# Optimization experiments

Measured on AMD Instinct MI355X. Metric: run time of the kernel, lower is better.

Reference implementation:

```python
import jax, jax.numpy as jnp
import numpy as np

D_MODEL = 512
KERNEL = 16
DILATIONS = (1, 1, 2, 2, 4, 4, 8, 8)
HEADS = len(DILATIONS)
HEAD_W = D_MODEL // HEADS
B, L = 2, 1024
MODE = "forward"  # causal: window sees only prior words


def setup_inputs() -> dict:
    key = jax.random.key(0)
    ks = jax.random.split(key, 8)
    s = 0.02  # small init like nn.Linear
    return {
        "tensor": jax.random.normal(ks[0], (B, L, D_MODEL), jnp.float32),
        "Wq": jax.random.normal(ks[1], (HEADS, HEAD_W, D_MODEL), jnp.float32) * s,
        "bq": jnp.zeros((HEADS, HEAD_W), jnp.float32),
        "Wk": jax.random.normal(ks[2], (HEADS, KERNEL, HEAD_W, D_MODEL), jnp.float32) * s,
        "bk": jnp.zeros((HEADS, KERNEL, HEAD_W), jnp.float32),
        "Wv": jax.random.normal(ks[3], (HEADS, KERNEL, HEAD_W, D_MODEL), jnp.float32) * s,
        "bv": jnp.zeros((HEADS, KERNEL, HEAD_W), jnp.float32),
        "Wo": jax.random.normal(ks[4], (D_MODEL, HEADS, HEAD_W), jnp.float32) * s,
        "bo": jnp.zeros((D_MODEL,), jnp.float32),
    }


def _window_indices():
    """Static gather indices replicating Glimpses.dilocal's dilated unfold.

    Returns idx of shape (H, L, K) indexing into a sequence zero-padded by
    max_off on both sides: content[h, l, k] = x_padded[idx[h, l, k]].
    """
    dil = np.asarray(DILATIONS)  # (H,)
    max_off = int((KERNEL - 1) * dil.max())
    if MODE == "forward":
        front = (KERNEL - 1) * dil           # all padding in front (causal)
    elif MODE == "backward":
        front = np.zeros_like(dil)           # all padding behind
    else:  # center
        front = ((KERNEL - 1) * dil) // 2
    l = np.arange(L)[None, :, None]
    k = np.arange(KERNEL)[None, None, :]
    d = dil[:, None, None]
    f = front[:, None, None]
    idx = l + k * d - f + max_off            # (H, L, K), always in-range
    return jnp.asarray(idx), max_off


_IDX, _MOFF = _window_indices()


def reference(tensor, Wq, bq, Wk, bk, Wv, bv, Wo, bo):
    # tensor: (B, L, D)
    xp = jnp.pad(tensor, ((0, 0), (_MOFF, _MOFF), (0, 0)))
    content = xp[:, _IDX, :]                                   # (B,H,L,K,D)
    # per-head query projection (kernel position 1)
    q = jnp.einsum('bld,hod->bhlo', tensor, Wq) + bq[:, None, :]        # (B,H,L,hw)
    # per-(head, kernel-position) independent key/value projections
    k = jnp.einsum('bhlkd,hkod->bhlko', content, Wk) + bk[:, None, :, :]
    v = jnp.einsum('bhlkd,hkod->bhlko', content, Wv) + bv[:, None, :, :]
    # tiny local attention over the K window positions
    logits = jnp.einsum('bhlo,bhlko->bhlk', q, k)               # (B,H,L,K)
    score = jax.nn.softmax(logits, axis=-1)
    # NOTE: original scales AFTER the score@value matmul (faithful to source)
    attn = jnp.einsum('bhlk,bhlko->bhlo', score, v)
    attn = attn / jnp.sqrt(jnp.asarray(HEAD_W, tensor.dtype))   # (B,H,L,hw)
    # dehead: merge (heads, head_width) -> d_model
    out = jnp.einsum('bhlo,dho->bld', attn, Wo) + bo            # (B,L,D)
    return out
```

## Files before the change

### kernel.cpp

```cpp
#include <hip/hip_runtime.h>


#define BD 2
#define LL 1024
#define DM 512
#define HH 8
#define KT 16
#define HW 64

#define NQKV 16896

typedef unsigned short u16;
typedef unsigned int u32;
typedef __bf16 bf16x8 __attribute__((ext_vector_type(8)));
typedef float f32x4 __attribute__((ext_vector_type(4)));
typedef unsigned short ushort4v __attribute__((ext_vector_type(4)));
typedef unsigned short ushort8v __attribute__((ext_vector_type(8)));

__constant__ int c_dil[8] = {1, 1, 2, 2, 4, 4, 8, 8};

__device__ __forceinline__ float bf2f(u16 u) {
    return __builtin_bit_cast(float, (u32)u << 16);
}
__device__ __forceinline__ u16 f2bf(float f) {
    u32 u = __builtin_bit_cast(u32, f);
    return (u16)((u + 0x7fffu + ((u >> 16) & 1u)) >> 16);
}

__device__ __forceinline__ void gl_lds16(const u16* g, u16* l) {
    __builtin_amdgcn_global_load_lds(
        (__attribute__((address_space(1))) void*)g,
        (__attribute__((address_space(3))) void*)l, 16, 0, 0);
}

__device__ __forceinline__ void bar() {
    asm volatile("" ::: "memory");
    __builtin_amdgcn_s_barrier();
    asm volatile("" ::: "memory");
}

__global__ __launch_bounds__(256, 3) void gemm_bf16(
    const u16* __restrict__ A, const u16* __restrict__ Bm,
    const float* __restrict__ bq, const float* __restrict__ bk,
    const float* __restrict__ bv,
    u16* __restrict__ qb, u16* __restrict__ kvb)
{
    const int bid = blockIdx.x;
    const int wg  = (bid & 7) * 264 + (bid >> 3);
    const int m0  = (wg & 15) << 7;
    const int n0  = (wg >> 4) << 7;

    __shared__ u16 As[3][128 * 32];
    __shared__ u16 Bs[3][128 * 32];

    const int tid  = threadIdx.x;
    const int wave = tid >> 6, lane = tid & 63;
    const int r0 = tid >> 2;
    const int cc = (tid & 3) << 3;
    const int mw = (wave >> 1) << 6;
    const int nw = (wave & 1) << 6;
    const int lr = lane & 15;
    const int qg = lane >> 4;
    const int ksw = ((qg ^ ((lr >> 1) & 3)) << 3);

    const u16* Ag = A  + (size_t)(m0 + r0) * DM + cc;
    const u16* Bg = Bm + (size_t)(n0 + r0) * DM + cc;
    u16* lA = &As[0][0] + tid * 8;
    u16* lB = &Bs[0][0] + tid * 8;

#define STG(t2, c) do {                                                    \
        const int ko_ = (t2) << 5;                                         \
        gl_lds16(Ag + ko_,                  lA + (c) * 4096);              \
        gl_lds16(Ag + ko_ + (size_t)64*DM,  lA + (c) * 4096 + 2048);       \
        gl_lds16(Bg + ko_,                  lB + (c) * 4096);              \
        gl_lds16(Bg + ko_ + (size_t)64*DM,  lB + (c) * 4096 + 2048);       \
    } while (0)

    f32x4 acc[4][4];
#pragma unroll
    for (int i = 0; i < 4; ++i)
#pragma unroll
        for (int j = 0; j < 4; ++j) acc[i][j] = (f32x4){0.f, 0.f, 0.f, 0.f};

    STG(0, 0);
    STG(1, 1);
    asm volatile("s_waitcnt vmcnt(4)" ::: "memory");
    bar();

#pragma unroll
    for (int t = 0; t < 16; ++t) {
        const int cur = t % 3;
        if (t < 14) STG(t + 2, (t + 2) % 3);

        bf16x8 af[4], bfr[4];
#pragma unroll
        for (int i = 0; i < 4; ++i)
            af[i] = *(const bf16x8*)&As[cur][(mw + (i << 4) + lr) * 32 + ksw];
#pragma unroll
        for (int j = 0; j < 4; ++j)
            bfr[j] = *(const bf16x8*)&Bs[cur][(nw + (j << 4) + lr) * 32 + ksw];
        __builtin_amdgcn_s_setprio(1);
#pragma unroll
        for (int i = 0; i < 4; ++i)
#pragma unroll
            for (int j = 0; j < 4; ++j)
                acc[i][j] = __builtin_amdgcn_mfma_f32_16x16x32_bf16(
                    af[i], bfr[j], acc[i][j], 0, 0, 0);
        __builtin_amdgcn_s_setprio(0);

        if (t < 14)
            asm volatile("s_waitcnt vmcnt(4)" ::: "memory");
        else if (t == 14)
            asm volatile("s_waitcnt vmcnt(0)" ::: "memory");
        if (t < 15) bar();
    }
#undef STG

    if (n0 < 512) {
#pragma unroll
        for (int i = 0; i < 4; ++i) {
            const int rowb = m0 + mw + (i << 4) + (qg << 2);
#pragma unroll
            for (int j = 0; j < 4; ++j) {
                const int col = n0 + nw + (j << 4) + lr;
                const float bs = bq[col];
#pragma unroll
                for (int r = 0; r < 4; ++r)
                    qb[(size_t)(rowb + r) * 512 + col] =
                        f2bf(acc[i][j][r] + bs);
            }
        }
    } else {
        const int reg = (n0 >= 8704);
        const float* bias = reg ? bv : bk;
        const int t0  = n0 - (reg ? 8704 : 512);
        const int h   = t0 >> 10;
        const int pb  = ((reg << 3) + h) << 4;
#pragma unroll
        for (int i = 0; i < 4; ++i) {
            const int rowb = m0 + mw + (i << 4) + (qg << 2);
#pragma unroll
            for (int j = 0; j < 4; ++j) {
                const int tcol  = (t0 & 1023) + nw + (j << 4) + lr;
                const int kslot = tcol >> 6;
                const int oo    = tcol & 63;
                const float bs  = bias[(h << 10) + tcol];
#pragma unroll
                for (int r = 0; r < 4; ++r) {
                    const int row = rowb + r;
                    const int bb  = row >> 10, l2 = row & 1023;
                    kvb[((size_t)(((pb + kslot) << 1) + bb) << 16)
                        + (l2 << 6) + oo] = f2bf(acc[i][j][r] + bs);
                }
            }
        }
    }
}

__global__ __launch_bounds__(256, 4) void gemm_out(
    const u16* __restrict__ A, const u16* __restrict__ Bm,
    const float* __restrict__ bias, float* __restrict__ C)
{
    __shared__ u16 As[3][64 * 32];
    __shared__ u16 Bs[3][64 * 32];

    const int tid  = threadIdx.x;
    const int wave = tid >> 6, lane = tid & 63;
    const int m0 = blockIdx.y << 6, n0 = blockIdx.x << 6;
    const int r0 = tid >> 2, cc = (tid & 3) << 3;
    const int mw = wave << 4;
    const int lr = lane & 15, qg = lane >> 4;
    const int ksw = ((qg ^ ((lr >> 1) & 3)) << 3);

    const u16* Ag = A  + (size_t)(m0 + r0) * DM + cc;
    const u16* Bg = Bm + (size_t)(n0 + r0) * DM + cc;
    u16* lA = &As[0][0] + tid * 8;
    u16* lB = &Bs[0][0] + tid * 8;

#define STG(t2, c) do {                                                    \
        const int ko_ = (t2) << 5;                                         \
        gl_lds16(Ag + ko_, lA + (c) * 2048);                               \
        gl_lds16(Bg + ko_, lB + (c) * 2048);                               \
    } while (0)

    f32x4 acc[4];
#pragma unroll
    for (int j = 0; j < 4; ++j) acc[j] = (f32x4){0.f, 0.f, 0.f, 0.f};

    STG(0, 0);
    STG(1, 1);
    asm volatile("s_waitcnt vmcnt(2)" ::: "memory");
    bar();

#pragma unroll
    for (int t = 0; t < 16; ++t) {
        const int cur = t % 3;
        if (t < 14) STG(t + 2, (t + 2) % 3);

        bf16x8 af = *(const bf16x8*)&As[cur][(mw + lr) * 32 + ksw];
        __builtin_amdgcn_s_setprio(1);
#pragma unroll
        for (int j = 0; j < 4; ++j) {
            bf16x8 bfr = *(const bf16x8*)&Bs[cur][((j << 4) + lr) * 32 + ksw];
            acc[j] = __builtin_amdgcn_mfma_f32_16x16x32_bf16(af, bfr, acc[j], 0, 0, 0);
        }
        __builtin_amdgcn_s_setprio(0);

        if (t < 14)
            asm volatile("s_waitcnt vmcnt(2)" ::: "memory");
        else if (t == 14)
            asm volatile("s_waitcnt vmcnt(0)" ::: "memory");
        if (t < 15) bar();
    }
#undef STG

#pragma unroll
    for (int j = 0; j < 4; ++j) {
        const int col = n0 + (j << 4) + lr;
        const float bs = bias[col];
#pragma unroll
        for (int r = 0; r < 4; ++r)
            C[(size_t)(m0 + mw + (qg << 2) + r) * DM + col] = acc[j][r] + bs;
    }
}

__global__ void cvt_swz(const float* __restrict__ x,  const float* __restrict__ Wq,
                        const float* __restrict__ Wk, const float* __restrict__ Wv,
                        const float* __restrict__ Wo,
                        u16* __restrict__ xb, u16* __restrict__ wb,
                        u16* __restrict__ wob)
{
    const int i = blockIdx.x * 256 + threadIdx.x;
    const float* src; u16* dst; int t;
    if (i < 131072) {
        t = i;
        src = x;  dst = xb;
    } else if (i < 1212416) {
        t = i - 131072;
        const int row = t >> 6;
        if      (row <  512) src = Wq;
        else if (row < 8704) src = Wk - (size_t)512 * DM;
        else                 src = Wv - (size_t)8704 * DM;
        dst = wb;
    } else {
        t = i - 1212416;
        src = Wo; dst = wob;
    }
    const int row = t >> 6;
    const int c8  = t & 63;
    const int s   = (row >> 1) & 3;
    const int oc  = (c8 & ~3) | ((c8 & 3) ^ s);
    const float* p = src + (size_t)row * DM + (oc << 3);
    float4 v0 = *(const float4*)p;
    float4 v1 = *(const float4*)(p + 4);
    ushort8v o = { f2bf(v0.x), f2bf(v0.y), f2bf(v0.z), f2bf(v0.w),
                   f2bf(v1.x), f2bf(v1.y), f2bf(v1.z), f2bf(v1.w) };
    *(ushort8v*)(dst + (size_t)row * DM + (c8 << 3)) = o;
}

__global__ __launch_bounds__(256, 4) void attn_bf16(
    const u16* __restrict__ qb,
    const u16* __restrict__ kvb,
    const float* __restrict__ bk,
    const float* __restrict__ bv,
    u16* __restrict__ attnb)
{
    const int tid = threadIdx.x;
    const int j   = tid & 7;
    const int ks  = (tid >> 3) & 1;
    const int ll  = tid >> 4;
    const int bid = blockIdx.x;
    const int h = bid & 7;
    const int t = (bid >> 3) & 63;
    const int b = bid >> 9;
    const int l = (t << 4) + ll;
    const int dil = c_dil[h];
    const int kof = ks << 3;

    const int hko = h * (KT * HW);

    float qf[8];
    {
        ushort8v qv = *(const ushort8v*)(qb + (size_t)(b * LL + l) * 512
                                         + h * HW + (j << 3));
#pragma unroll
        for (int z = 0; z < 8; ++z) qf[z] = bf2f(qv[z]);
    }

    const u16* kbase = kvb + ((size_t)(((h << 4) << 1) + b) << 16) + (j << 3);
    const u16* vbase = kbase + ((size_t)(8 << 4) << 17);

    ushort8v kr[8];
#pragma unroll
    for (int kk = 0; kk < 8; ++kk) {
        const int k = kof + kk;
        const int src = l - (KT - 1 - k) * dil;
        if (src >= 0)
            kr[kk] = *(const ushort8v*)(kbase + ((size_t)k << 17) + (src << 6));
    }

    float lg[8];
#pragma unroll
    for (int kk = 0; kk < 8; ++kk) {
        const int k = kof + kk;
        const int src = l - (KT - 1 - k) * dil;
        float p = 0.f;
        if (src >= 0) {
#pragma unroll
            for (int z = 0; z < 8; ++z) p += qf[z] * bf2f(kr[kk][z]);
        } else {
            const float* bkp = bk + hko + k * HW + (j << 3);
#pragma unroll
            for (int z = 0; z < 8; ++z) p += qf[z] * bkp[z];
        }
        p += __shfl_xor(p, 1);
        p += __shfl_xor(p, 2);
        p += __shfl_xor(p, 4);
        lg[kk] = p;
    }

    float m = lg[0];
#pragma unroll
    for (int kk = 1; kk < 8; ++kk) m = fmaxf(m, lg[kk]);
    m = fmaxf(m, __shfl_xor(m, 8));
    float s = 0.f;
#pragma unroll
    for (int kk = 0; kk < 8; ++kk) { lg[kk] = __expf(lg[kk] - m); s += lg[kk]; }
    s += __shfl_xor(s, 8);
    const float inv = 1.f / s;

    ushort8v vr[8];
#pragma unroll
    for (int kk = 0; kk < 8; ++kk) {
        const int k = kof + kk;
        const int src = l - (KT - 1 - k) * dil;
        if (src >= 0)
            vr[kk] = *(const ushort8v*)(vbase + ((size_t)k << 17) + (src << 6));
    }

    float acc[8];
#pragma unroll
    for (int z = 0; z < 8; ++z) acc[z] = 0.f;
#pragma unroll
    for (int kk = 0; kk < 8; ++kk) {
        const int k = kof + kk;
        const int src = l - (KT - 1 - k) * dil;
        const float sc = lg[kk] * inv;
        if (src >= 0) {
#pragma unroll
            for (int z = 0; z < 8; ++z) acc[z] = fmaf(sc, bf2f(vr[kk][z]), acc[z]);
        } else {
            const float* bvp = bv + hko + k * HW + (j << 3);
#pragma unroll
            for (int z = 0; z < 8; ++z) acc[z] = fmaf(sc, bvp[z], acc[z]);
        }
    }

#pragma unroll
    for (int z = 0; z < 8; ++z) acc[z] += __shfl_xor(acc[z], 8);

    if (ks == 0) {
        ushort8v o;
#pragma unroll
        for (int z = 0; z < 8; ++z) o[z] = f2bf(acc[z] * 0.125f);
        const int row = b * LL + l;
        const int k8 = h * 8 + j;
        const int sw = ((k8 & 3) ^ ((l >> 1) & 3)) << 3;
        *(ushort8v*)(attnb + (size_t)row * DM + ((k8 >> 2) << 5) + sw) = o;
    }
}

__global__ __launch_bounds__(256, 2) void gemm_nt_bias(
    const float* __restrict__ A, const float* __restrict__ Bm,
    const float* __restrict__ bias, float* __restrict__ C,
    int M, int N, int Kd)
{
    __shared__ float As[16][68];
    __shared__ float Bs[16][68];
    const int tid = threadIdx.x;
    const int tx = tid & 15, ty = tid >> 4;
    const int r0 = blockIdx.y << 6, c0 = blockIdx.x << 6;
    const int lr = tid >> 2, k4 = (tid & 3) << 2;
    const float* Ap = A  + (size_t)(r0 + lr) * Kd + k4;
    const float* Bp = Bm + (size_t)(c0 + lr) * Kd + k4;
    float acc[4][4];
#pragma unroll
    for (int i = 0; i < 4; ++i)
#pragma unroll
        for (int j = 0; j < 4; ++j) acc[i][j] = 0.f;
    for (int d0 = 0; d0 < Kd; d0 += 16) {
        float4 av = *(const float4*)(Ap + d0);
        float4 bv = *(const float4*)(Bp + d0);
        As[k4 + 0][lr] = av.x; As[k4 + 1][lr] = av.y;
        As[k4 + 2][lr] = av.z; As[k4 + 3][lr] = av.w;
        Bs[k4 + 0][lr] = bv.x; Bs[k4 + 1][lr] = bv.y;
        Bs[k4 + 2][lr] = bv.z; Bs[k4 + 3][lr] = bv.w;
        __syncthreads();
#pragma unroll
        for (int dd = 0; dd < 16; ++dd) {
            float4 a4 = *(const float4*)&As[dd][ty << 2];
            float4 b4 = *(const float4*)&Bs[dd][tx << 2];
            float ar[4] = {a4.x, a4.y, a4.z, a4.w};
            float br[4] = {b4.x, b4.y, b4.z, b4.w};
#pragma unroll
            for (int i = 0; i < 4; ++i)
#pragma unroll
                for (int j = 0; j < 4; ++j)
                    acc[i][j] = fmaf(ar[i], br[j], acc[i][j]);
        }
        __syncthreads();
    }
#pragma unroll
    for (int i = 0; i < 4; ++i) {
        float4 o;
        const int c = c0 + (tx << 2);
        o.x = acc[i][0] + bias[c + 0];
        o.y = acc[i][1] + bias[c + 1];
        o.z = acc[i][2] + bias[c + 2];
        o.w = acc[i][3] + bias[c + 3];
        *(float4*)&C[(size_t)(r0 + (ty << 2) + i) * N + c] = o;
    }
}

__device__ __forceinline__ void tile_gemm_f32(
    const float* __restrict__ xb, int src, bool ok,
    const float* __restrict__ wrow,
    int lr, int k4, int tx, int ty,
    float (&As)[16][68], float (&Ws)[16][68], float (&acc)[4][4])
{
#pragma unroll
    for (int i = 0; i < 4; ++i)
#pragma unroll
        for (int j = 0; j < 4; ++j) acc[i][j] = 0.f;
    const float* xrow = xb + (size_t)(ok ? src : 0) * DM + k4;
    for (int d0 = 0; d0 < DM; d0 += 16) {
        float4 av = make_float4(0.f, 0.f, 0.f, 0.f);
        if (ok) av = *(const float4*)(xrow + d0);
        float4 wv = *(const float4*)(wrow + d0);
        As[k4 + 0][lr] = av.x; As[k4 + 1][lr] = av.y;
        As[k4 + 2][lr] = av.z; As[k4 + 3][lr] = av.w;
        Ws[k4 + 0][lr] = wv.x; Ws[k4 + 1][lr] = wv.y;
        Ws[k4 + 2][lr] = wv.z; Ws[k4 + 3][lr] = wv.w;
        __syncthreads();
#pragma unroll
        for (int dd = 0; dd < 16; ++dd) {
            float4 a4 = *(const float4*)&As[dd][ty << 2];
            float4 b4 = *(const float4*)&Ws[dd][tx << 2];
            float ar[4] = {a4.x, a4.y, a4.z, a4.w};
            float br[4] = {b4.x, b4.y, b4.z, b4.w};
#pragma unroll
            for (int i = 0; i < 4; ++i)
#pragma unroll
                for (int j = 0; j < 4; ++j)
                    acc[i][j] = fmaf(ar[i], br[j], acc[i][j]);
        }
        __syncthreads();
    }
}

__global__ __launch_bounds__(256, 2) void attn_kernel(
    const float* __restrict__ x, const float* __restrict__ q,
    const float* __restrict__ Wk, const float* __restrict__ bk,
    const float* __restrict__ Wv, const float* __restrict__ bv,
    float* __restrict__ attn)
{
    __shared__ float As[16][68];
    __shared__ float Ws[16][68];
    __shared__ float qs[64][68];
    __shared__ float lg[64][17];
    __shared__ float red[64][17];
    const int tid = threadIdx.x;
    const int tx = tid & 15, ty = tid >> 4;
    const int bid = blockIdx.x;
    const int h = bid & 7, t = (bid >> 3) & 15, b = bid >> 7;
    const int l0 = t << 6;
    const int dil = c_dil[h];
    const int lr = tid >> 2, k4 = (tid & 3) << 2;
    for (int i = tid; i < 64 * 16; i += 256) {
        int l = i >> 4, o4 = (i & 15) << 2;
        float4 v = *(const float4*)&q[((size_t)(b * LL + l0 + l) * HH + h) * HW + o4];
        *(float4*)&qs[l][o4] = v;
    }
    const float* xb  = x  + (size_t)b * LL * DM;
    const float* Wkh = Wk + (size_t)h * KT * HW * DM;
    const float* Wvh = Wv + (size_t)h * KT * HW * DM;
    const float* bkh = bk + h * KT * HW;
    const float* bvh = bv + h * KT * HW;
    float acc[4][4];
    for (int kk = 0; kk < KT; ++kk) {
        const int src = l0 + lr - (KT - 1 - kk) * dil;
        const bool ok = (src >= 0) && (src < LL);
        tile_gemm_f32(xb, src, ok, Wkh + (size_t)(kk * HW + lr) * DM + k4,
                      lr, k4, tx, ty, As, Ws, acc);
        const float* bkp = bkh + kk * HW + (tx << 2);
#pragma unroll
        for (int i = 0; i < 4; ++i) {
            float p = 0.f;
#pragma unroll
            for (int j = 0; j < 4; ++j)
                p += (acc[i][j] + bkp[j]) * qs[(ty << 2) + i][(tx << 2) + j];
            red[(ty << 2) + i][tx] = p;
        }
        __syncthreads();
        if (tid < 64) {
            float s = 0.f;
#pragma unroll
            for (int u = 0; u < 16; ++u) s += red[tid][u];
            lg[tid][kk] = s;
        }
        __syncthreads();
    }
    if (tid < 64) {
        float m = lg[tid][0];
#pragma unroll
        for (int u = 1; u < KT; ++u) m = fmaxf(m, lg[tid][u]);
        float s = 0.f;
#pragma unroll
        for (int u = 0; u < KT; ++u) {
            float e = expf(lg[tid][u] - m);
            lg[tid][u] = e; s += e;
        }
        float inv = 1.f / s;
#pragma unroll
        for (int u = 0; u < KT; ++u) lg[tid][u] *= inv;
    }
    __syncthreads();
    float vacc[4][4];
#pragma unroll
    for (int i = 0; i < 4; ++i)
#pragma unroll
        for (int j = 0; j < 4; ++j) vacc[i][j] = 0.f;
    for (int kk = 0; kk < KT; ++kk) {
        const int src = l0 + lr - (KT - 1 - kk) * dil;
        const bool ok = (src >= 0) && (src < LL);
        tile_gemm_f32(xb, src, ok, Wvh + (size_t)(kk * HW + lr) * DM + k4,
                      lr, k4, tx, ty, As, Ws, acc);
        const float* bvp = bvh + kk * HW + (tx << 2);
#pragma unroll
        for (int i = 0; i < 4; ++i) {
            float sc = lg[(ty << 2) + i][kk];
#pragma unroll
            for (int j = 0; j < 4; ++j)
                vacc[i][j] = fmaf(sc, acc[i][j] + bvp[j], vacc[i][j]);
        }
    }
#pragma unroll
    for (int i = 0; i < 4; ++i) {
        float4 o;
        o.x = vacc[i][0] * 0.125f;
        o.y = vacc[i][1] * 0.125f;
        o.z = vacc[i][2] * 0.125f;
        o.w = vacc[i][3] * 0.125f;
        *(float4*)&attn[((size_t)(b * LL + l0 + (ty << 2) + i) * HH + h) * HW + (tx << 2)] = o;
    }
}

extern "C" void kernel_launch(void* const* d_in, const int* in_sizes, int n_in,
                              void* d_out, int out_size, void* d_ws, size_t ws_size,
                              hipStream_t stream)
{
    const float* x  = (const float*)d_in[0];
    const float* Wq = (const float*)d_in[1];
    const float* bq = (const float*)d_in[2];
    const float* Wk = (const float*)d_in[3];
    const float* bk = (const float*)d_in[4];
    const float* Wv = (const float*)d_in[5];
    const float* bv = (const float*)d_in[6];
    const float* Wo = (const float*)d_in[7];
    const float* bo = (const float*)d_in[8];
    float* out = (float*)d_out;

    const int M = BD * LL;

    const size_t N_X   = (size_t)BD * LL * DM;
    const size_t N_WB  = (size_t)NQKV * DM;
    const size_t N_WO  = (size_t)DM * DM;
    const size_t N_QKV = (size_t)M * NQKV;
    const size_t NEED  = (N_X + N_WB + N_WO + N_QKV + N_X) * 2;

    if (ws_size >= NEED) {
        u16* xb    = (u16*)d_ws;
        u16* wb    = xb    + N_X;
        u16* wob   = wb    + N_WB;
        u16* qb    = wob   + N_WO;
        u16* kvb   = qb    + N_X;
        u16* attnb = qb    + N_QKV;

        cvt_swz<<<4864, 256, 0, stream>>>(x, Wq, Wk, Wv, Wo, xb, wb, wob);

        gemm_bf16<<<dim3(2112), 256, 0, stream>>>(
            xb, wb, bq, bk, bv, qb, kvb);

        attn_bf16<<<BD * HH * (LL / 16), 256, 0, stream>>>(
            qb, kvb, bk, bv, attnb);

        gemm_out<<<dim3(8, 32), 256, 0, stream>>>(attnb, wob, bo, out);
    } else {
        float* qws = (float*)d_ws;
        float* aws = qws + (size_t)BD * LL * HH * HW;
        gemm_nt_bias<<<dim3((HH * HW) / 64, M / 64), 256, 0, stream>>>(
            x, Wq, bq, qws, M, HH * HW, DM);
        attn_kernel<<<BD * HH * (LL / 64), 256, 0, stream>>>(
            x, qws, Wk, bk, Wv, bv, aws);
        gemm_nt_bias<<<dim3(DM / 64, M / 64), 256, 0, stream>>>(
            aws, Wo, bo, out, M, DM, HH * HW);
    }
}
```

Measured before the change: 161.9 us.

## Enlarge QKV GEMM tiles to 256x256 with 8 waves and interleaved prefetch

Result: slower. 175.6 us (+8.4%).

```diff
diff --git a/kernel.cpp b/kernel.cpp
--- a/kernel.cpp
+++ b/kernel.cpp
@@ -39,95 +39,120 @@
     asm volatile("" ::: "memory");
 }
 
-__global__ __launch_bounds__(256, 3) void gemm_bf16(
+__global__ __launch_bounds__(512, 1) void gemm_bf16(
     const u16* __restrict__ A, const u16* __restrict__ Bm,
     const float* __restrict__ bq, const float* __restrict__ bk,
     const float* __restrict__ bv,
     u16* __restrict__ qb, u16* __restrict__ kvb)
 {
     const int bid = blockIdx.x;
-    const int wg  = (bid & 7) * 264 + (bid >> 3);
-    const int m0  = (wg & 15) << 7;
-    const int n0  = (wg >> 4) << 7;
-
-    __shared__ u16 As[3][128 * 32];
-    __shared__ u16 Bs[3][128 * 32];
-
-    const int tid  = threadIdx.x;
-    const int wave = tid >> 6, lane = tid & 63;
+    const int wg  = (bid & 7) * 66 + (bid >> 3);
+    const int m0  = (wg & 7) << 8;
+    const int n0  = (wg >> 3) << 8;
+
+    __shared__ u16 As[2][2][256 * 32];
+    __shared__ u16 Bs[2][2][256 * 32];
+
+    const int tid = threadIdx.x;
+    const int wid = tid >> 6, lane = tid & 63;
+    const int wm  = wid >> 2;
+    const int wn  = wid & 3;
+    const int lr  = lane & 15, qg = lane >> 4;
+    const int ksw = ((qg ^ ((lr >> 1) & 3)) << 3);
+
     const int r0 = tid >> 2;
     const int cc = (tid & 3) << 3;
-    const int mw = (wave >> 1) << 6;
-    const int nw = (wave & 1) << 6;
-    const int lr = lane & 15;
-    const int qg = lane >> 4;
-    const int ksw = ((qg ^ ((lr >> 1) & 3)) << 3);
-
     const u16* Ag = A  + (size_t)(m0 + r0) * DM + cc;
     const u16* Bg = Bm + (size_t)(n0 + r0) * DM + cc;
-    u16* lA = &As[0][0] + tid * 8;
-    u16* lB = &Bs[0][0] + tid * 8;
-
-#define STG(t2, c) do {                                                    \
-        const int ko_ = (t2) << 5;                                         \
-        gl_lds16(Ag + ko_,                  lA + (c) * 4096);              \
-        gl_lds16(Ag + ko_ + (size_t)64*DM,  lA + (c) * 4096 + 2048);       \
-        gl_lds16(Bg + ko_,                  lB + (c) * 4096);              \
-        gl_lds16(Bg + ko_ + (size_t)64*DM,  lB + (c) * 4096 + 2048);       \
+    u16* lA = &As[0][0][0] + tid * 8;
+    u16* lB = &Bs[0][0][0] + tid * 8;
+
+#define STGA(kt, b, th) do {                                               \
+        gl_lds16(Ag + (size_t)(th) * 128 * DM + ((kt) << 6),               \
+                 lA + (((b) * 2 + 0) * 256 + (th) * 128) * 32);            \
+        gl_lds16(Ag + (size_t)(th) * 128 * DM + ((kt) << 6) + 32,          \
+                 lA + (((b) * 2 + 1) * 256 + (th) * 128) * 32);            \
     } while (0)
-
-    f32x4 acc[4][4];
-#pragma unroll
-    for (int i = 0; i < 4; ++i)
+#define STGB(kt, b, th) do {                                               \
+        gl_lds16(Bg + (size_t)(th) * 128 * DM + ((kt) << 6),               \
+                 lB + (((b) * 2 + 0) * 256 + (th) * 128) * 32);            \
+        gl_lds16(Bg + (size_t)(th) * 128 * DM + ((kt) << 6) + 32,          \
+                 lB + (((b) * 2 + 1) * 256 + (th) * 128) * 32);            \
+    } while (0)
+
+    f32x4 acc[8][4];
+#pragma unroll
+    for (int i = 0; i < 8; ++i)
 #pragma unroll
         for (int j = 0; j < 4; ++j) acc[i][j] = (f32x4){0.f, 0.f, 0.f, 0.f};
 
-    STG(0, 0);
-    STG(1, 1);
-    asm volatile("s_waitcnt vmcnt(4)" ::: "memory");
+    STGA(0, 0, 0); STGA(0, 0, 1); STGB(0, 0, 0); STGB(0, 0, 1);
+    asm volatile("s_waitcnt vmcnt(0)" ::: "memory");
     bar();
 
 #pragma unroll
-    for (int t = 0; t < 16; ++t) {
-        const int cur = t % 3;
-        if (t < 14) STG(t + 2, (t + 2) % 3);
-
-        bf16x8 af[4], bfr[4];
-#pragma unroll
-        for (int i = 0; i < 4; ++i)
-            af[i] = *(const bf16x8*)&As[cur][(mw + (i << 4) + lr) * 32 + ksw];
-#pragma unroll
-        for (int j = 0; j < 4; ++j)
-            bfr[j] = *(const bf16x8*)&Bs[cur][(nw + (j << 4) + lr) * 32 + ksw];
-        __builtin_amdgcn_s_setprio(1);
-#pragma unroll
-        for (int i = 0; i < 4; ++i)
-#pragma unroll
-            for (int j = 0; j < 4; ++j)
-                acc[i][j] = __builtin_amdgcn_mfma_f32_16x16x32_bf16(
-                    af[i], bfr[j], acc[i][j], 0, 0, 0);
-        __builtin_amdgcn_s_setprio(0);
-
-        if (t < 14)
-            asm volatile("s_waitcnt vmcnt(4)" ::: "memory");
-        else if (t == 14)
-            asm volatile("s_waitcnt vmcnt(0)" ::: "memory");
-        if (t < 15) bar();
-    }
-#undef STG
+    for (int it = 0; it < 4; ++it) {
+#pragma unroll
+        for (int hf = 0; hf < 2; ++hf) {
+#pragma unroll
+            for (int ph = 0; ph < 4; ++ph) {
+                const int mh = ph >> 1, ks = ph & 1;
+
+                bf16x8 af[4], bfr[4];
+#pragma unroll
+                for (int mi = 0; mi < 4; ++mi)
+                    af[mi] = *(const bf16x8*)
+                        &As[hf][ks][((wm << 7) + ((mh * 4 + mi) << 4) + lr)
+                                    * 32 + ksw];
+#pragma unroll
+                for (int nf = 0; nf < 4; ++nf)
+                    bfr[nf] = *(const bf16x8*)
+                        &Bs[hf][ks][((wn << 6) + (nf << 4) + lr) * 32 + ksw];
+
+                if (hf == 0) {
+                    if      (ph == 0) STGA(2 * it + 1, 1, 0);
+                    else if (ph == 1) STGA(2 * it + 1, 1, 1);
+                    else if (ph == 2) STGB(2 * it + 1, 1, 0);
+                    else              STGB(2 * it + 1, 1, 1);
+                } else if (it < 3) {
+                    if      (ph == 0) STGA(2 * it + 2, 0, 0);
+                    else if (ph == 1) STGA(2 * it + 2, 0, 1);
+                    else if (ph == 2) STGB(2 * it + 2, 0, 0);
+                    else              STGB(2 * it + 2, 0, 1);
+                }
+
+                __builtin_amdgcn_s_setprio(1);
+#pragma unroll
+                for (int mi = 0; mi < 4; ++mi)
+#pragma unroll
+                    for (int nf = 0; nf < 4; ++nf)
+                        acc[mh * 4 + mi][nf] =
+                            __builtin_amdgcn_mfma_f32_16x16x32_bf16(
+                                af[mi], bfr[nf], acc[mh * 4 + mi][nf],
+                                0, 0, 0);
+                __builtin_amdgcn_s_setprio(0);
+
+                if (ph == 3 && !(it == 3 && hf == 1))
+                    asm volatile("s_waitcnt vmcnt(0)" ::: "memory");
+                bar();
+            }
+        }
+    }
+#undef STGA
+#undef STGB
 
     if (n0 < 512) {
 #pragma unroll
-        for (int i = 0; i < 4; ++i) {
-            const int rowb = m0 + mw + (i << 4) + (qg << 2);
-#pragma unroll
-            for (int j = 0; j < 4; ++j) {
-                const int col = n0 + nw + (j << 4) + lr;
+        for (int mf = 0; mf < 8; ++mf) {
+            const int rowb = m0 + (wm << 7) + (mf << 4) + (qg << 2);
+#pragma unroll
+            for (int nf = 0; nf < 4; ++nf) {
+                const int col = n0 + (wn << 6) + (nf << 4) + lr;
                 const float bs = bq[col];
 #pragma unroll
                 for (int r = 0; r < 4; ++r)
                     qb[(size_t)(rowb + r) * 512 + col] =
-                        f2bf(acc[i][j][r] + bs);
+                        f2bf(acc[mf][nf][r] + bs);
             }
         }
     } else {
@@ -137,11 +162,11 @@
         const int h   = t0 >> 10;
         const int pb  = ((reg << 3) + h) << 4;
 #pragma unroll
-        for (int i = 0; i < 4; ++i) {
-            const int rowb = m0 + mw + (i << 4) + (qg << 2);
-#pragma unroll
-            for (int j = 0; j < 4; ++j) {
-                const int tcol  = (t0 & 1023) + nw + (j << 4) + lr;
+        for (int mf = 0; mf < 8; ++mf) {
+            const int rowb = m0 + (wm << 7) + (mf << 4) + (qg << 2);
+#pragma unroll
+            for (int nf = 0; nf < 4; ++nf) {
+                const int tcol  = (t0 & 1023) + (wn << 6) + (nf << 4) + lr;
                 const int kslot = tcol >> 6;
                 const int oo    = tcol & 63;
                 const float bs  = bias[(h << 10) + tcol];
@@ -150,7 +175,7 @@
                     const int row = rowb + r;
                     const int bb  = row >> 10, l2 = row & 1023;
                     kvb[((size_t)(((pb + kslot) << 1) + bb) << 16)
-                        + (l2 << 6) + oo] = f2bf(acc[i][j][r] + bs);
+                        + (l2 << 6) + oo] = f2bf(acc[mf][nf][r] + bs);
                 }
             }
         }
@@ -588,7 +613,7 @@
 
         cvt_swz<<<4864, 256, 0, stream>>>(x, Wq, Wk, Wv, Wo, xb, wb, wob);
 
-        gemm_bf16<<<dim3(2112), 256, 0, stream>>>(
+        gemm_bf16<<<dim3(528), 512, 0, stream>>>(
             xb, wb, bq, bk, bv, qb, kvb);
 
         attn_bf16<<<BD * HH * (LL / 16), 256, 0, stream>>>(
```
